# Kernel tuning notes

Hardware: AMD Instinct MI355X
Metric: run time of the kernel (lower is better)

Reference implementation:

```python
import jax, jax.numpy as jnp
import numpy as np
from jax import lax

EPS = 1e-5

def conv2d(x, w, pad):
    # x: NCHW, w: OIHW
    return lax.conv_general_dilated(x, w, (1, 1), [(pad, pad), (pad, pad)],
                                    dimension_numbers=('NCHW', 'OIHW', 'NCHW'))

def batchnorm(x, gamma, beta):
    # training-mode BN: batch statistics over N,H,W (biased variance, as torch)
    m = jnp.mean(x, axis=(0, 2, 3), keepdims=True)
    v = jnp.var(x, axis=(0, 2, 3), keepdims=True)
    g = gamma.reshape(1, -1, 1, 1)
    b = beta.reshape(1, -1, 1, 1)
    return (x - m) * jax.lax.rsqrt(v + EPS) * g + b

def setup_inputs() -> dict:
    key = jax.random.key(0)
    ks = jax.random.split(key, 8)
    B, Cin, Cmid, NC, H, W = 4, 2048, 512, 19, 64, 64
    s = lambda fan: (2.0 / fan) ** 0.5
    return {
        'x':  jax.random.normal(ks[0], (B, Cin, H, W), jnp.float32),
        'Wa': jax.random.normal(ks[1], (Cmid, Cin, 3, 3), jnp.float32) * s(Cin * 9),
        'ga': jnp.ones((Cmid,), jnp.float32),
        'ba': jnp.zeros((Cmid,), jnp.float32),
        'Wb': jax.random.normal(ks[2], (Cmid, Cmid, 1, 1), jnp.float32) * s(Cmid),
        'bb': jnp.zeros((Cmid,), jnp.float32),
        'W1': jax.random.normal(ks[3], (Cmid, Cin + Cmid, 3, 3), jnp.float32) * s((Cin + Cmid) * 9),
        'g1': jnp.ones((Cmid,), jnp.float32),
        'b1': jnp.zeros((Cmid,), jnp.float32),
        'W4': jax.random.normal(ks[4], (NC, Cmid, 1, 1), jnp.float32) * s(Cmid),
        'b4': jnp.zeros((NC,), jnp.float32),
    }

def reference(x, Wa, ga, ba, Wb, bb, W1, g1, b1, W4, b4):
    # conva: 3x3 conv (no bias) -> BN -> ReLU
    out = jax.nn.relu(batchnorm(conv2d(x, Wa, 1), ga, ba))
    # convb: 1x1 conv with bias
    out = conv2d(out, Wb, 0) + bb.reshape(1, -1, 1, 1)
    # concat input with projected features along channels
    out = jnp.concatenate([x, out], axis=1)  # [B, Cin+Cmid, H, W]
    # b1 (3x3, no bias) -> b2 BN -> b3 ReLU
    out = jax.nn.relu(batchnorm(conv2d(out, W1, 1), g1, b1))
    # b4: 1x1 classifier conv with bias
    out_final = conv2d(out, W4, 0) + b4.reshape(1, -1, 1, 1)
    return (out, out_final)
```

## Files before the change

kernel.cpp:

```cpp
#include <hip/hip_runtime.h>

typedef unsigned short ushort_t;
typedef unsigned int uint_t;
typedef unsigned long long ulong_t;

typedef __bf16 bf16x8 __attribute__((ext_vector_type(8)));
typedef float f32x4 __attribute__((ext_vector_type(4)));
typedef float f32x16 __attribute__((ext_vector_type(16)));
typedef unsigned short u16x4 __attribute__((ext_vector_type(4)));

#define DEV __device__ __forceinline__
#define SB() __builtin_amdgcn_sched_barrier(0)
#define WAITV(n) asm volatile("s_waitcnt vmcnt(" #n ")" ::: "memory")

DEV ushort_t f2bf(float x) {
  uint_t u = __float_as_uint(x);
  u += 0x7fffu + ((u >> 16) & 1u);
  return (ushort_t)(u >> 16);
}
DEV float bf2f(ushort_t h) { return __uint_as_float(((uint_t)h) << 16); }

DEV void gload16(ulong_t g, const void* l) {
  __builtin_amdgcn_global_load_lds(
      (__attribute__((address_space(1))) void*)g,
      (__attribute__((address_space(3))) void*)(void*)l,
      16, 0, 0);
}
DEV int nxt3(int x) { return x == 2 ? 0 : x + 1; }

__global__ void zero_k(float* __restrict__ p, int n) {
  int i = blockIdx.x * 256 + threadIdx.x;
  if (i < n) p[i] = 0.f;
}

__global__ __launch_bounds__(256) void cvt_x_k(const float* __restrict__ X,
                                               ushort_t* __restrict__ P) {
  __shared__ float T[64][65];
  const int t = threadIdx.x;
  const int p0 = blockIdx.x * 64;
  const int c0 = blockIdx.y * 64;
  const int b = p0 >> 12;
  const int pin0 = p0 & 4095;
#pragma unroll
  for (int it = 0; it < 4; ++it) {
    const int cl = it * 16 + (t >> 4);
    const int pl = (t & 15) * 4;
    const f32x4 v = *(const f32x4*)&X[((size_t)(b * 2048 + c0 + cl)) * 4096 + pin0 + pl];
#pragma unroll
    for (int j = 0; j < 4; ++j) T[cl][pl + j] = v[j];
  }
  __syncthreads();
#pragma unroll
  for (int it = 0; it < 4; ++it) {
    const int pl = it * 16 + (t >> 4);
    const int cl = (t & 15) * 4;
    u16x4 h, l;
#pragma unroll
    for (int j = 0; j < 4; ++j) {
      float v = T[cl + j][pl];
      ushort_t hh = f2bf(v);
      h[j] = hh;
      l[j] = f2bf(v - bf2f(hh));
    }
    const int c = c0 + cl;
    const size_t o = (size_t)(p0 + pl) * 4096 + (size_t)((c >> 5) << 6) + (c & 31);
    *(u16x4*)&P[o] = h;
    *(u16x4*)&P[o + 32] = l;
  }
}

__global__ __launch_bounds__(256) void cvt_w3n_k(const float* __restrict__ W,
                                                 ushort_t* __restrict__ P,
                                                 int I, int O) {
  const int t = threadIdx.x;
  const int o = blockIdx.y;
  const int i = blockIdx.x * 256 + t;
  const float* src = W + ((size_t)o * I + i) * 9;
  const int cb = i >> 5;
  const int kk = (i >> 4) & 1, kh = (i >> 3) & 1, e = i & 7;
  const int cg = o >> 5;
  const int lane = kh * 32 + (o & 31);
#pragma unroll
  for (int j = 0; j < 9; ++j) {
    const float v = src[j];
    const ushort_t h = f2bf(v);
    const size_t b16 = ((((size_t)(cb * 9 + j) * 16 + cg) * 2 + 0) * 2 + kk) * 64 + lane;
    P[b16 * 8 + e] = h;
    P[(b16 + 128) * 8 + e] = f2bf(v - bf2f(h));
  }
}

__global__ __launch_bounds__(256) void cvt_e_k(const float* __restrict__ W,
                                               ushort_t* __restrict__ P) {
  int i = blockIdx.x * 256 + threadIdx.x;
  float v = W[i];
  ushort_t h = f2bf(v);
  const int o = i >> 9, ic = i & 511;
  const size_t d = (size_t)o * 1024 + (size_t)((ic >> 5) << 6) + (ic & 31);
  P[d] = h;
  P[d + 32] = f2bf(v - bf2f(h));
}

__global__ __launch_bounds__(256) void stats_k(const float* __restrict__ X,
                                               float* __restrict__ S,
                                               float* __restrict__ Q) {
  const int t = threadIdx.x;
  const int r0 = blockIdx.x * 32;
  const int c = t * 2;
  float s0 = 0, s1 = 0, q0 = 0, q1 = 0;
  for (int r = 0; r < 32; ++r) {
    const float2 v = *(const float2*)&X[((size_t)(r0 + r)) * 512 + c];
    s0 += v.x; s1 += v.y;
    q0 += v.x * v.x; q1 += v.y * v.y;
  }
  atomicAdd(&S[c], s0); atomicAdd(&S[c + 1], s1);
  atomicAdd(&Q[c], q0); atomicAdd(&Q[c + 1], q1);
}

__global__ void bnparams_k(const float* __restrict__ S, const float* __restrict__ Q,
                           const float* __restrict__ g, const float* __restrict__ b,
                           float* __restrict__ sc, float* __restrict__ sh) {
  const int t = threadIdx.x;
  const float m = S[t] * (1.0f / 16384.0f);
  const float v = Q[t] * (1.0f / 16384.0f) - m * m;
  const float inv = rsqrtf(v + 1e-5f);
  const float s = g[t] * inv;
  sc[t] = s;
  sh[t] = b[t] - m * s;
}

__global__ __launch_bounds__(256) void bnact_k(const float* __restrict__ X,
                                               const float* __restrict__ sc,
                                               const float* __restrict__ sh,
                                               ushort_t* __restrict__ P) {
  const size_t i0 = ((size_t)blockIdx.x * 256 + threadIdx.x) * 16;
  const int c0 = (int)(i0 & 511);
  const size_t px = i0 >> 9;
#pragma unroll
  for (int q = 0; q < 4; ++q) {
    const f32x4 v = *(const f32x4*)&X[i0 + q * 4];
    const f32x4 s = *(const f32x4*)&sc[c0 + q * 4];
    const f32x4 d = *(const f32x4*)&sh[c0 + q * 4];
    u16x4 h, l;
#pragma unroll
    for (int j = 0; j < 4; ++j) {
      float y = fmaf(v[j], s[j], d[j]);
      y = fmaxf(y, 0.f);
      ushort_t hh = f2bf(y);
      h[j] = hh;
      l[j] = f2bf(y - bf2f(hh));
    }
    const int c = c0 + q * 4;
    const size_t o = px * 1024 + (size_t)((c >> 5) << 6) + (c & 31);
    *(u16x4*)&P[o] = h;
    *(u16x4*)&P[o + 32] = l;
  }
}

__global__ __launch_bounds__(256) void bn_nchw_k(const float* __restrict__ X,
                                                 const float* __restrict__ sc,
                                                 const float* __restrict__ sh,
                                                 float* __restrict__ O) {
  __shared__ float T[64][65];
  const int t = threadIdx.x;
  const int p0 = blockIdx.x * 64;
  const int c0 = blockIdx.y * 64;
  const int b = p0 >> 12, pin0 = p0 & 4095;
#pragma unroll
  for (int it = 0; it < 4; ++it) {
    const int pl = it * 16 + (t >> 4);
    const int cl = (t & 15) * 4;
    const f32x4 v = *(const f32x4*)&X[((size_t)(p0 + pl)) * 512 + c0 + cl];
#pragma unroll
    for (int j = 0; j < 4; ++j) {
      float y = fmaf(v[j], sc[c0 + cl + j], sh[c0 + cl + j]);
      T[pl][cl + j] = fmaxf(y, 0.f);
    }
  }
  __syncthreads();
#pragma unroll
  for (int it = 0; it < 4; ++it) {
    const int cl = it * 16 + (t >> 4);
    const int pl = (t & 15) * 4;
    f32x4 o;
#pragma unroll
    for (int j = 0; j < 4; ++j) o[j] = T[pl + j][cl];
    *(f32x4*)&O[((size_t)(b * 512 + c0 + cl)) * 4096 + pin0 + pl] = o;
  }
}

__global__ __launch_bounds__(256) void conv4_k(const float* __restrict__ X,
                                               const float* __restrict__ sc,
                                               const float* __restrict__ sh,
                                               const float* __restrict__ W4,
                                               const float* __restrict__ B4,
                                               float* __restrict__ O) {
  __shared__ float A[256][69];
  __shared__ float WL[64][19];
  const int t = threadIdx.x;
  const int g0 = blockIdx.x * 256;
  float acc[19];
#pragma unroll
  for (int n = 0; n < 19; ++n) acc[n] = 0.f;
  for (int kc = 0; kc < 8; ++kc) {
    const int k0 = kc * 64;
    __syncthreads();
#pragma unroll
    for (int it = 0; it < 16; ++it) {
      const int rl = it * 16 + (t >> 4);
      const int cl = (t & 15) * 4;
      const f32x4 v = *(const f32x4*)&X[((size_t)(g0 + rl)) * 512 + k0 + cl];
#pragma unroll
      for (int j = 0; j < 4; ++j)
        A[rl][cl + j] = fmaxf(fmaf(v[j], sc[k0 + cl + j], sh[k0 + cl + j]), 0.f);
    }
    for (int e = t; e < 1216; e += 256) {
      int k = e / 19, n = e - k * 19;
      WL[k][n] = W4[(size_t)n * 512 + k0 + k];
    }
    __syncthreads();
#pragma unroll 8
    for (int k = 0; k < 64; ++k) {
      const float a = A[t][k];
#pragma unroll
      for (int n = 0; n < 19; ++n) acc[n] = fmaf(a, WL[k][n], acc[n]);
    }
  }
  const int g = g0 + t;
  const int b = g >> 12, pin = g & 4095;
#pragma unroll
  for (int n = 0; n < 19; ++n)
    O[((size_t)(b * 19 + n)) * 4096 + pin] = acc[n] + B4[n];
}

__global__ __launch_bounds__(512, 2) void conv9dual_k(
    const ushort_t* __restrict__ A1, int S1,
    const ushort_t* __restrict__ WA, const ushort_t* __restrict__ WC,
    int CBt, const ushort_t* __restrict__ zp,
    float* __restrict__ CoA, float* __restrict__ CoC) {
  constexpr int RW = 6;
  constexpr int SPD = 24;
  constexpr int AI = 6;
  constexpr int APL = 24576;
  constexpr int ABUF = 49152;
  __shared__ char Ald[2 * ABUF];
  const int t = threadIdx.x, lane = t & 63, wid = t >> 6;
  const int wr = wid >> 1, wc = wid & 1;
  const int gid = blockIdx.x, xcd = gid & 7, k_ = gid >> 3;
  const int by = xcd * 8 + (k_ & 7), bx = k_ >> 3;
  const int b = by >> 4, r0 = (by & 15) * 4, bbase = b * 4096;
  const int pxl = lane & 31;
  const int khalf = lane >> 5;
  const int lofs = lane * 16;
  const int row0 = by * 256 + wr * 64;
  const int col0 = bx * 128 + wc * 64;
  const int rb = 4 * khalf;

  auto stageAslice = [&](int cb, int bufA, int i) {
    const int g = wid * AI + i;
    const int d = g / SPD, rem = g - d * SPD;
    const int pxb = rem >> 1, kk = rem & 1;
    const int p = pxb * 32 + pxl;
    const int irow = r0 + (p >> 6) - 1;
    const int gpx = bbase + irow * 64 + (p & 63);
    const ulong_t el = (ulong_t)gpx * (uint_t)S1 +
                       (uint_t)(cb * 64 + d * 32 + (kk * 2 + khalf) * 8);
    const bool oob = (unsigned)irow >= 64u;
    const ulong_t src = oob ? (ulong_t)(zp + lane * 8) : (ulong_t)(A1 + el);
    gload16(src, Ald + bufA + d * APL + (pxb * 2 + kk) * 1024);
  };

  struct BS { bf16x8 b[2][2][2]; };
  auto loadB = [&](BS& s, const ushort_t* W, int cs, int tap) {
#pragma unroll
    for (int ni = 0; ni < 2; ++ni)
#pragma unroll
      for (int kk = 0; kk < 2; ++kk)
#pragma unroll
        for (int dt = 0; dt < 2; ++dt) {
          const size_t b16 =
              ((((size_t)(cs * 9 + tap) * 16 + (bx * 4 + wc * 2 + ni)) * 2 + dt) * 2 + kk) * 64 + lane;
          s.b[ni][kk][dt] = *(const bf16x8*)(W + b16 * 8);
        }
  };

  f32x16 accA[2][2], accC[2][2];
#pragma unroll
  for (int i = 0; i < 2; ++i)
#pragma unroll
    for (int j2 = 0; j2 < 2; ++j2) {
      accA[i][j2] = (f32x16){0.f};
      accC[i][j2] = (f32x16){0.f};
    }

  auto mfmaBlk = [&](f32x16 (&acc)[2][2], const bf16x8 (&a)[2][2][2], const BS& s) {
    __builtin_amdgcn_s_setprio(1);
#pragma unroll
    for (int kk = 0; kk < 2; ++kk) {
#pragma unroll
      for (int mi = 0; mi < 2; ++mi)
#pragma unroll
        for (int ni = 0; ni < 2; ++ni)
          acc[mi][ni] = __builtin_amdgcn_mfma_f32_32x32x16_bf16(
              a[mi][kk][0], s.b[ni][kk][0], acc[mi][ni], 0, 0, 0);
#pragma unroll
      for (int mi = 0; mi < 2; ++mi)
#pragma unroll
        for (int ni = 0; ni < 2; ++ni)
          acc[mi][ni] = __builtin_amdgcn_mfma_f32_32x32x16_bf16(
              a[mi][kk][0], s.b[ni][kk][1], acc[mi][ni], 0, 0, 0);
#pragma unroll
      for (int mi = 0; mi < 2; ++mi)
#pragma unroll
        for (int ni = 0; ni < 2; ++ni)
          acc[mi][ni] = __builtin_amdgcn_mfma_f32_32x32x16_bf16(
              a[mi][kk][1], s.b[ni][kk][0], acc[mi][ni], 0, 0, 0);
    }
    __builtin_amdgcn_s_setprio(0);
  };

#pragma unroll
  for (int i = 0; i < AI; ++i) stageAslice(0, 0, i);
  WAITV(0);
  SB();
  __builtin_amdgcn_s_barrier();
  SB();

  for (int cs = 0; cs < CBt; ++cs) {
    const int ab = (cs & 1) * ABUF;
    const int nb = ((cs + 1) & 1) * ABUF;
#pragma unroll
    for (int tap = 0; tap < 9; ++tap) {
      BS wa;
      loadB(wa, WA, cs, tap);
      if (tap < AI && cs + 1 < CBt) stageAslice(cs + 1, nb, tap);
      const int prow = wr + tap / 3, dx = tap % 3 - 1;
      const char* Ab = Ald + ab;
      bf16x8 a[2][2][2];
#pragma unroll
      for (int mi = 0; mi < 2; ++mi) {
        const int pb0 = prow * 2 + mi;
        int ao0;
        if (dx == 0) {
          ao0 = pb0 * 2048 + lofs;
        } else {
          int px = pb0 * 32 + pxl + dx;
          px = px < 0 ? 0 : (px > RW * 64 - 1 ? RW * 64 - 1 : px);
          ao0 = (px >> 5) * 2048 + khalf * 512 + (px & 31) * 16;
        }
#pragma unroll
        for (int kk = 0; kk < 2; ++kk) {
          const int ao = ao0 + kk * 1024;
          a[mi][kk][0] = *(const bf16x8*)(Ab + ao);
          a[mi][kk][1] = *(const bf16x8*)(Ab + APL + ao);
        }
      }
      if (dx == -1 && pxl == 0) {
        bf16x8 z = {};
        a[0][0][0] = z; a[0][0][1] = z; a[0][1][0] = z; a[0][1][1] = z;
      }
      if (dx == 1 && pxl == 31) {
        bf16x8 z = {};
        a[1][0][0] = z; a[1][0][1] = z; a[1][1][0] = z; a[1][1][1] = z;
      }
      mfmaBlk(accA, a, wa);
      SB();
      BS wcs;
      loadB(wcs, WC, cs, tap);
      mfmaBlk(accC, a, wcs);
    }
    WAITV(0);
    SB();
    __builtin_amdgcn_s_barrier();
    SB();
  }

#pragma unroll
  for (int mi = 0; mi < 2; ++mi)
#pragma unroll
    for (int ni = 0; ni < 2; ++ni) {
      const int c = col0 + ni * 32 + pxl;
#pragma unroll
      for (int rg = 0; rg < 16; ++rg) {
        const int r = row0 + mi * 32 + (rg & 3) + 8 * (rg >> 2) + rb;
        CoA[(size_t)r * 512 + c] = accA[mi][ni][rg];
        CoC[(size_t)r * 512 + c] = accC[mi][ni][rg];
      }
    }
}

template <int AINIT>
__global__ __launch_bounds__(512, 2) void conv9_k(
    const ushort_t* __restrict__ A1, int S1,
    const ushort_t* __restrict__ WB, int CBt, int cbOff,
    const ushort_t* __restrict__ zp,
    float* __restrict__ Co) {
  constexpr int RW = 6;
  constexpr int SPD = 24;
  constexpr int AI = 6;
  constexpr int APL = 24576;
  constexpr int ABUF = 49152;
  __shared__ char Ald[2 * ABUF];
  const int t = threadIdx.x, lane = t & 63, wid = t >> 6;
  const int wr = wid >> 1, wc = wid & 1;
  const int gid = blockIdx.x, xcd = gid & 7, k_ = gid >> 3;
  const int by = xcd * 8 + (k_ & 7), bx = k_ >> 3;
  const int b = by >> 4, r0 = (by & 15) * 4, bbase = b * 4096;
  const int pxl = lane & 31;
  const int khalf = lane >> 5;
  const int lofs = lane * 16;
  const int row0 = by * 256 + wr * 64;
  const int col0 = bx * 128 + wc * 64;
  const int rb = 4 * khalf;

  auto stageAslice = [&](int cb, int bufA, int i) {
    const int g = wid * AI + i;
    const int d = g / SPD, rem = g - d * SPD;
    const int pxb = rem >> 1, kk = rem & 1;
    const int p = pxb * 32 + pxl;
    const int irow = r0 + (p >> 6) - 1;
    const int gpx = bbase + irow * 64 + (p & 63);
    const ulong_t el = (ulong_t)gpx * (uint_t)S1 +
                       (uint_t)(cb * 64 + d * 32 + (kk * 2 + khalf) * 8);
    const bool oob = (unsigned)irow >= 64u;
    const ulong_t src = oob ? (ulong_t)(zp + lane * 8) : (ulong_t)(A1 + el);
    gload16(src, Ald + bufA + d * APL + (pxb * 2 + kk) * 1024);
  };

  struct BS { bf16x8 b[2][2][2]; };
  auto loadB = [&](BS& s, int cs, int tap) {
#pragma unroll
    for (int ni = 0; ni < 2; ++ni)
#pragma unroll
      for (int kk = 0; kk < 2; ++kk)
#pragma unroll
        for (int dt = 0; dt < 2; ++dt) {
          const size_t b16 =
              ((((size_t)((cs + cbOff) * 9 + tap) * 16 + (bx * 4 + wc * 2 + ni)) * 2 + dt) * 2 + kk) * 64 + lane;
          s.b[ni][kk][dt] = *(const bf16x8*)(WB + b16 * 8);
        }
  };

  f32x16 acc[2][2];
  if constexpr (AINIT) {
#pragma unroll
    for (int mi = 0; mi < 2; ++mi)
#pragma unroll
      for (int ni = 0; ni < 2; ++ni) {
        const int c = col0 + ni * 32 + pxl;
#pragma unroll
        for (int rg = 0; rg < 16; ++rg) {
          const int r = row0 + mi * 32 + (rg & 3) + 8 * (rg >> 2) + rb;
          acc[mi][ni][rg] = Co[(size_t)r * 512 + c];
        }
      }
  } else {
#pragma unroll
    for (int i = 0; i < 2; ++i)
#pragma unroll
      for (int j2 = 0; j2 < 2; ++j2) acc[i][j2] = (f32x16){0.f};
  }

#pragma unroll
  for (int i = 0; i < AI; ++i) stageAslice(0, 0, i);
  WAITV(0);
  SB();
  __builtin_amdgcn_s_barrier();
  SB();

  for (int cs = 0; cs < CBt; ++cs) {
    const int ab = (cs & 1) * ABUF;
    const int nb = ((cs + 1) & 1) * ABUF;
#pragma unroll
    for (int tap = 0; tap < 9; ++tap) {
      BS wa;
      loadB(wa, cs, tap);
      if (tap < AI && cs + 1 < CBt) stageAslice(cs + 1, nb, tap);
      const int prow = wr + tap / 3, dx = tap % 3 - 1;
      const char* Ab = Ald + ab;
      bf16x8 a[2][2][2];
#pragma unroll
      for (int mi = 0; mi < 2; ++mi) {
        const int pb0 = prow * 2 + mi;
        int ao0;
        if (dx == 0) {
          ao0 = pb0 * 2048 + lofs;
        } else {
          int px = pb0 * 32 + pxl + dx;
          px = px < 0 ? 0 : (px > RW * 64 - 1 ? RW * 64 - 1 : px);
          ao0 = (px >> 5) * 2048 + khalf * 512 + (px & 31) * 16;
        }
#pragma unroll
        for (int kk = 0; kk < 2; ++kk) {
          const int ao = ao0 + kk * 1024;
          a[mi][kk][0] = *(const bf16x8*)(Ab + ao);
          a[mi][kk][1] = *(const bf16x8*)(Ab + APL + ao);
        }
      }
      if (dx == -1 && pxl == 0) {
        bf16x8 z = {};
        a[0][0][0] = z; a[0][0][1] = z; a[0][1][0] = z; a[0][1][1] = z;
      }
      if (dx == 1 && pxl == 31) {
        bf16x8 z = {};
        a[1][0][0] = z; a[1][0][1] = z; a[1][1][0] = z; a[1][1][1] = z;
      }
      __builtin_amdgcn_s_setprio(1);
#pragma unroll
      for (int kk = 0; kk < 2; ++kk) {
#pragma unroll
        for (int mi = 0; mi < 2; ++mi)
#pragma unroll
          for (int ni = 0; ni < 2; ++ni)
            acc[mi][ni] = __builtin_amdgcn_mfma_f32_32x32x16_bf16(
                a[mi][kk][0], wa.b[ni][kk][0], acc[mi][ni], 0, 0, 0);
#pragma unroll
        for (int mi = 0; mi < 2; ++mi)
#pragma unroll
          for (int ni = 0; ni < 2; ++ni)
            acc[mi][ni] = __builtin_amdgcn_mfma_f32_32x32x16_bf16(
                a[mi][kk][0], wa.b[ni][kk][1], acc[mi][ni], 0, 0, 0);
#pragma unroll
        for (int mi = 0; mi < 2; ++mi)
#pragma unroll
          for (int ni = 0; ni < 2; ++ni)
            acc[mi][ni] = __builtin_amdgcn_mfma_f32_32x32x16_bf16(
                a[mi][kk][1], wa.b[ni][kk][0], acc[mi][ni], 0, 0, 0);
      }
      __builtin_amdgcn_s_setprio(0);
    }
    WAITV(0);
    SB();
    __builtin_amdgcn_s_barrier();
    SB();
  }

#pragma unroll
  for (int mi = 0; mi < 2; ++mi)
#pragma unroll
    for (int ni = 0; ni < 2; ++ni) {
      const int c = col0 + ni * 32 + pxl;
#pragma unroll
      for (int rg = 0; rg < 16; ++rg) {
        const int r = row0 + mi * 32 + (rg & 3) + 8 * (rg >> 2) + rb;
        Co[(size_t)r * 512 + c] = acc[mi][ni][rg];
      }
    }
}

__global__ __launch_bounds__(512, 2) void conv1x1_k(
    const ushort_t* __restrict__ A1, int S1,
    const ushort_t* __restrict__ WB, int CBt, int NBS,
    const ushort_t* __restrict__ zp,
    ushort_t* __restrict__ Cp, const float* __restrict__ bias) {
  constexpr int SPD = 16;
  constexpr int AI = 4;
  constexpr int APL = 16384;
  constexpr int ABUF = 32768;
  __shared__ char lds_all[147456];
  char* Ald = lds_all;
  char* Bld = lds_all + 98304;
  const int t = threadIdx.x, lane = t & 63, wid = t >> 6;
  const int wr = wid >> 1, wc = wid & 1;
  const int gid = blockIdx.x, xcd = gid & 7, k_ = gid >> 3;
  const int by = xcd * 8 + (k_ & 7), bx = k_ >> 3;
  const int b = by >> 4, r0 = (by & 15) * 4, bbase = b * 4096;
  const int pxl = lane & 31;
  const int khalf = lane >> 5;
  const int lofs = lane * 16;

  auto stageA = [&](int cb, int bufA) {
#pragma unroll
    for (int i = 0; i < AI; ++i) {
      const int g = wid * AI + i;
      const int d = g / SPD, rem = g - d * SPD;
      const int pxb = rem >> 1, kk = rem & 1;
      const int p = pxb * 32 + pxl;
      const int irow = r0 + (p >> 6);
      const int gpx = bbase + irow * 64 + (p & 63);
      const ulong_t el = (ulong_t)gpx * (uint_t)S1 +
                         (uint_t)(cb * 64 + d * 32 + (kk * 2 + khalf) * 8);
      gload16((ulong_t)(A1 + el), Ald + bufA + d * APL + (pxb * 2 + kk) * 1024);
    }
  };
  auto stageB = [&](int cb, int bufB) {
#pragma unroll
    for (int q = 0; q < 2; ++q) {
      const int s = wid * 2 + q;
      const int d = s >> 3, rem = s & 7, cob = rem >> 1, kk = rem & 1;
      const int co = bx * 128 + cob * 32 + pxl;
      const ulong_t el = (ulong_t)co * (uint_t)NBS +
                         (uint_t)(cb * 64 + d * 32 + (kk * 2 + khalf) * 8);
      gload16((ulong_t)(WB + el), Bld + bufB + d * 8192 + (cob * 2 + kk) * 1024);
    }
  };

  f32x16 acc[2][2];
#pragma unroll
  for (int i = 0; i < 2; ++i)
#pragma unroll
    for (int j2 = 0; j2 < 2; ++j2) acc[i][j2] = (f32x16){0.f};

  auto compute = [&](int abufB, int bbufB) {
    const char* Ab = Ald + abufB;
    const char* Bb = Bld + bbufB;
    bf16x8 a[2][2][2], bf[2][2][2];
#pragma unroll
    for (int ni = 0; ni < 2; ++ni)
#pragma unroll
      for (int kk = 0; kk < 2; ++kk) {
        const int bo = (wc * 2 + ni) * 2048 + kk * 1024 + lofs;
        bf[ni][kk][0] = *(const bf16x8*)(Bb + bo);
        bf[ni][kk][1] = *(const bf16x8*)(Bb + 8192 + bo);
      }
#pragma unroll
    for (int mi = 0; mi < 2; ++mi) {
      const int ao0 = ((wr * 2 + mi)) * 2048 + lofs;
#pragma unroll
      for (int kk = 0; kk < 2; ++kk) {
        const int ao = ao0 + kk * 1024;
        a[mi][kk][0] = *(const bf16x8*)(Ab + ao);
        a[mi][kk][1] = *(const bf16x8*)(Ab + APL + ao);
      }
    }
#pragma unroll
    for (int kk = 0; kk < 2; ++kk) {
#pragma unroll
      for (int mi = 0; mi < 2; ++mi)
#pragma unroll
        for (int ni = 0; ni < 2; ++ni)
          acc[mi][ni] = __builtin_amdgcn_mfma_f32_32x32x16_bf16(
              a[mi][kk][0], bf[ni][kk][0], acc[mi][ni], 0, 0, 0);
#pragma unroll
      for (int mi = 0; mi < 2; ++mi)
#pragma unroll
        for (int ni = 0; ni < 2; ++ni)
          acc[mi][ni] = __builtin_amdgcn_mfma_f32_32x32x16_bf16(
              a[mi][kk][0], bf[ni][kk][1], acc[mi][ni], 0, 0, 0);
#pragma unroll
      for (int mi = 0; mi < 2; ++mi)
#pragma unroll
        for (int ni = 0; ni < 2; ++ni)
          acc[mi][ni] = __builtin_amdgcn_mfma_f32_32x32x16_bf16(
              a[mi][kk][1], bf[ni][kk][0], acc[mi][ni], 0, 0, 0);
    }
  };

  int rr = 0;
  stageA(0, 0);
  stageB(0, 0);
  SB();
  stageA(1, ABUF);
  stageB(1, 16384);
  for (int cs = 0; cs < CBt; ++cs) {
    SB();
    WAITV(6);
    SB();
    __builtin_amdgcn_s_barrier();
    SB();
    const int rr2 = nxt3(nxt3(rr));
    if (cs + 2 < CBt) {
      stageA(cs + 2, rr2 * ABUF);
      stageB(cs + 2, rr2 * 16384);
    }
    compute(rr * ABUF, rr * 16384);
    rr = nxt3(rr);
  }

  const int row0 = by * 256 + wr * 64;
  const int col0 = bx * 128 + wc * 64;
  const int rb = 4 * khalf;
#pragma unroll
  for (int ni = 0; ni < 2; ++ni) {
    const int c = col0 + ni * 32 + pxl;
    const float bv = bias[c];
    const size_t cg = (size_t)((c >> 5) << 6) + (c & 31);
#pragma unroll
    for (int mi = 0; mi < 2; ++mi)
#pragma unroll
      for (int rg = 0; rg < 16; ++rg) {
        const int r = row0 + mi * 32 + (rg & 3) + 8 * (rg >> 2) + rb;
        const float v = acc[mi][ni][rg] + bv;
        const ushort_t h = f2bf(v);
        Cp[(size_t)r * 1024 + cg] = h;
        Cp[(size_t)r * 1024 + cg + 32] = f2bf(v - bf2f(h));
      }
  }
}

extern "C" void kernel_launch(void* const* d_in, const int* in_sizes, int n_in,
                              void* d_out, int out_size, void* d_ws, size_t ws_size,
                              hipStream_t stream) {
  const float* x  = (const float*)d_in[0];
  const float* Wa = (const float*)d_in[1];
  const float* ga = (const float*)d_in[2];
  const float* ba = (const float*)d_in[3];
  const float* Wb = (const float*)d_in[4];
  const float* bb = (const float*)d_in[5];
  const float* W1 = (const float*)d_in[6];
  const float* g1 = (const float*)d_in[7];
  const float* b1 = (const float*)d_in[8];
  const float* W4 = (const float*)d_in[9];
  const float* b4 = (const float*)d_in[10];
  float* out0 = (float*)d_out;
  float* outF = out0 + (size_t)4 * 512 * 64 * 64;

  char* ws = (char*)d_ws;
  size_t off = 0;
  auto take = [&](size_t bytes) -> char* {
    char* p = ws + off;
    off += (bytes + 255) & ~(size_t)255;
    return p;
  };
  const size_t PAD = 16384;
  ushort_t* zp  = (ushort_t*)take(8192);
  float* sumA = (float*)take(2048);
  float* ssA  = (float*)take(2048);
  float* scA  = (float*)take(2048);
  float* shA  = (float*)take(2048);
  float* sum1 = (float*)take(2048);
  float* ss1  = (float*)take(2048);
  float* sc1  = (float*)take(2048);
  float* sh1  = (float*)take(2048);
  ushort_t* X2  = (ushort_t*)take((size_t)16384 * 4096 * 2 + PAD);
  ushort_t* WA2 = (ushort_t*)take((size_t)9 * 512 * 4096 * 2 + PAD);
  ushort_t* W12 = (ushort_t*)take((size_t)9 * 512 * 5120 * 2 + PAD);
  ushort_t* WBb = (ushort_t*)take((size_t)512 * 1024 * 2 + PAD);
  ushort_t* oA2 = (ushort_t*)take((size_t)16384 * 1024 * 2 + PAD);
  ushort_t* oB2 = (ushort_t*)take((size_t)16384 * 1024 * 2 + PAD);
  float* convaRaw = (float*)take((size_t)16384 * 512 * 4);
  float* conv1Raw = (float*)take((size_t)16384 * 512 * 4);
  if (ws_size < off) return;

  zero_k<<<dim3(24), dim3(256), 0, stream>>>((float*)ws, 6144);
  cvt_x_k<<<dim3(256, 32), dim3(256), 0, stream>>>(x, X2);
  cvt_w3n_k<<<dim3(8, 512), dim3(256), 0, stream>>>(Wa, WA2, 2048, 512);
  cvt_w3n_k<<<dim3(10, 512), dim3(256), 0, stream>>>(W1, W12, 2560, 512);
  cvt_e_k<<<dim3(1024), dim3(256), 0, stream>>>(Wb, WBb);

  conv9dual_k<<<dim3(256), dim3(512), 0, stream>>>(
      X2, 4096, WA2, W12, 64, zp, convaRaw, conv1Raw);

  stats_k<<<dim3(512), dim3(256), 0, stream>>>(convaRaw, sumA, ssA);
  bnparams_k<<<dim3(1), dim3(512), 0, stream>>>(sumA, ssA, ga, ba, scA, shA);
  bnact_k<<<dim3(2048), dim3(256), 0, stream>>>(convaRaw, scA, shA, oA2);

  conv1x1_k<<<dim3(256), dim3(512), 0, stream>>>(
      oA2, 1024, WBb, 16, 1024, zp, oB2, bb);

  conv9_k<1><<<dim3(256), dim3(512), 0, stream>>>(
      oB2, 1024, W12, 16, 64, zp, conv1Raw);

  stats_k<<<dim3(512), dim3(256), 0, stream>>>(conv1Raw, sum1, ss1);
  bnparams_k<<<dim3(1), dim3(512), 0, stream>>>(sum1, ss1, g1, b1, sc1, sh1);

  bn_nchw_k<<<dim3(256, 8), dim3(256), 0, stream>>>(conv1Raw, sc1, sh1, out0);
  conv4_k<<<dim3(64), dim3(256), 0, stream>>>(conv1Raw, sc1, sh1, W4, b4, outF);
}
```

Baseline: 1.972 ms.

## Split dual 3x3 conv reduction across two K-halves with partial-sum buffers

```diff
diff --git a/kernel.cpp b/kernel.cpp
--- a/kernel.cpp
+++ b/kernel.cpp
@@ -101,6 +101,26 @@
   P[d + 32] = f2bf(v - bf2f(h));
 }
 
+__global__ __launch_bounds__(256) void stats2_k(const float* __restrict__ X0,
+                                                const float* __restrict__ X1,
+                                                float* __restrict__ S,
+                                                float* __restrict__ Q) {
+  const int t = threadIdx.x;
+  const int r0 = blockIdx.x * 32;
+  const int c = t * 2;
+  float s0 = 0, s1 = 0, q0 = 0, q1 = 0;
+  for (int r = 0; r < 32; ++r) {
+    const size_t o = ((size_t)(r0 + r)) * 512 + c;
+    const float2 a = *(const float2*)&X0[o];
+    const float2 b = *(const float2*)&X1[o];
+    const float vx = a.x + b.x, vy = a.y + b.y;
+    s0 += vx; s1 += vy;
+    q0 += vx * vx; q1 += vy * vy;
+  }
+  atomicAdd(&S[c], s0); atomicAdd(&S[c + 1], s1);
+  atomicAdd(&Q[c], q0); atomicAdd(&Q[c + 1], q1);
+}
+
 __global__ __launch_bounds__(256) void stats_k(const float* __restrict__ X,
                                                float* __restrict__ S,
                                                float* __restrict__ Q) {
@@ -129,22 +149,24 @@
   sh[t] = b[t] - m * s;
 }
 
-__global__ __launch_bounds__(256) void bnact_k(const float* __restrict__ X,
-                                               const float* __restrict__ sc,
-                                               const float* __restrict__ sh,
-                                               ushort_t* __restrict__ P) {
+__global__ __launch_bounds__(256) void bnact2_k(const float* __restrict__ X0,
+                                                const float* __restrict__ X1,
+                                                const float* __restrict__ sc,
+                                                const float* __restrict__ sh,
+                                                ushort_t* __restrict__ P) {
   const size_t i0 = ((size_t)blockIdx.x * 256 + threadIdx.x) * 16;
   const int c0 = (int)(i0 & 511);
   const size_t px = i0 >> 9;
 #pragma unroll
   for (int q = 0; q < 4; ++q) {
-    const f32x4 v = *(const f32x4*)&X[i0 + q * 4];
+    const f32x4 v0 = *(const f32x4*)&X0[i0 + q * 4];
+    const f32x4 v1 = *(const f32x4*)&X1[i0 + q * 4];
     const f32x4 s = *(const f32x4*)&sc[c0 + q * 4];
     const f32x4 d = *(const f32x4*)&sh[c0 + q * 4];
     u16x4 h, l;
 #pragma unroll
     for (int j = 0; j < 4; ++j) {
-      float y = fmaf(v[j], s[j], d[j]);
+      float y = fmaf(v0[j] + v1[j], s[j], d[j]);
       y = fmaxf(y, 0.f);
       ushort_t hh = f2bf(y);
       h[j] = hh;
@@ -236,18 +258,19 @@
 __global__ __launch_bounds__(512, 2) void conv9dual_k(
     const ushort_t* __restrict__ A1, int S1,
     const ushort_t* __restrict__ WA, const ushort_t* __restrict__ WC,
-    int CBt, const ushort_t* __restrict__ zp,
-    float* __restrict__ CoA, float* __restrict__ CoC) {
+    const ushort_t* __restrict__ zp,
+    float* __restrict__ CoA0, float* __restrict__ CoA1,
+    float* __restrict__ CoC0, float* __restrict__ CoC1) {
   constexpr int RW = 6;
   constexpr int SPD = 24;
   constexpr int AI = 6;
   constexpr int APL = 24576;
-  constexpr int ABUF = 49152;
-  __shared__ char Ald[2 * ABUF];
+  __shared__ char Ald[49152];
   const int t = threadIdx.x, lane = t & 63, wid = t >> 6;
   const int wr = wid >> 1, wc = wid & 1;
   const int gid = blockIdx.x, xcd = gid & 7, k_ = gid >> 3;
-  const int by = xcd * 8 + (k_ & 7), bx = k_ >> 3;
+  const int by = xcd * 8 + (k_ & 7), bx = (k_ >> 3) & 3, kh = k_ >> 5;
+  const int cs0 = kh * 32, cs1 = cs0 + 32;
   const int b = by >> 4, r0 = (by & 15) * 4, bbase = b * 4096;
   const int pxl = lane & 31;
   const int khalf = lane >> 5;
@@ -255,8 +278,10 @@
   const int row0 = by * 256 + wr * 64;
   const int col0 = bx * 128 + wc * 64;
   const int rb = 4 * khalf;
-
-  auto stageAslice = [&](int cb, int bufA, int i) {
+  float* __restrict__ CoA = kh ? CoA1 : CoA0;
+  float* __restrict__ CoC = kh ? CoC1 : CoC0;
+
+  auto stageAslice = [&](int cb, int i) {
     const int g = wid * AI + i;
     const int d = g / SPD, rem = g - d * SPD;
     const int pxb = rem >> 1, kk = rem & 1;
@@ -267,7 +292,7 @@
                        (uint_t)(cb * 64 + d * 32 + (kk * 2 + khalf) * 8);
     const bool oob = (unsigned)irow >= 64u;
     const ulong_t src = oob ? (ulong_t)(zp + lane * 8) : (ulong_t)(A1 + el);
-    gload16(src, Ald + bufA + d * APL + (pxb * 2 + kk) * 1024);
+    gload16(src, Ald + d * APL + (pxb * 2 + kk) * 1024);
   };
 
   struct BS { bf16x8 b[2][2][2]; };
@@ -320,22 +345,18 @@
   };
 
 #pragma unroll
-  for (int i = 0; i < AI; ++i) stageAslice(0, 0, i);
+  for (int i = 0; i < AI; ++i) stageAslice(cs0, i);
   WAITV(0);
   SB();
   __builtin_amdgcn_s_barrier();
   SB();
 
-  for (int cs = 0; cs < CBt; ++cs) {
-    const int ab = (cs & 1) * ABUF;
-    const int nb = ((cs + 1) & 1) * ABUF;
+  for (int cs = cs0; cs < cs1; ++cs) {
 #pragma unroll
     for (int tap = 0; tap < 9; ++tap) {
       BS wa;
       loadB(wa, WA, cs, tap);
-      if (tap < AI && cs + 1 < CBt) stageAslice(cs + 1, nb, tap);
       const int prow = wr + tap / 3, dx = tap % 3 - 1;
-      const char* Ab = Ald + ab;
       bf16x8 a[2][2][2];
 #pragma unroll
       for (int mi = 0; mi < 2; ++mi) {
@@ -351,8 +372,8 @@
 #pragma unroll
         for (int kk = 0; kk < 2; ++kk) {
           const int ao = ao0 + kk * 1024;
-          a[mi][kk][0] = *(const bf16x8*)(Ab + ao);
-          a[mi][kk][1] = *(const bf16x8*)(Ab + APL + ao);
+          a[mi][kk][0] = *(const bf16x8*)(Ald + ao);
+          a[mi][kk][1] = *(const bf16x8*)(Ald + APL + ao);
         }
       }
       if (dx == -1 && pxl == 0) {
@@ -369,6 +390,13 @@
       loadB(wcs, WC, cs, tap);
       mfmaBlk(accC, a, wcs);
     }
+    SB();
+    __builtin_amdgcn_s_barrier();
+    SB();
+    if (cs + 1 < cs1) {
+#pragma unroll
+      for (int i = 0; i < AI; ++i) stageAslice(cs + 1, i);
+    }
     WAITV(0);
     SB();
     __builtin_amdgcn_s_barrier();
@@ -389,11 +417,11 @@
     }
 }
 
-template <int AINIT>
 __global__ __launch_bounds__(512, 2) void conv9_k(
     const ushort_t* __restrict__ A1, int S1,
     const ushort_t* __restrict__ WB, int CBt, int cbOff,
     const ushort_t* __restrict__ zp,
+    const float* __restrict__ P0, const float* __restrict__ P1,
     float* __restrict__ Co) {
   constexpr int RW = 6;
   constexpr int SPD = 24;
@@ -442,24 +470,17 @@
   };
 
   f32x16 acc[2][2];
-  if constexpr (AINIT) {
-#pragma unroll
-    for (int mi = 0; mi < 2; ++mi)
-#pragma unroll
-      for (int ni = 0; ni < 2; ++ni) {
-        const int c = col0 + ni * 32 + pxl;
-#pragma unroll
-        for (int rg = 0; rg < 16; ++rg) {
-          const int r = row0 + mi * 32 + (rg & 3) + 8 * (rg >> 2) + rb;
-          acc[mi][ni][rg] = Co[(size_t)r * 512 + c];
-        }
-      }
-  } else {
-#pragma unroll
-    for (int i = 0; i < 2; ++i)
-#pragma unroll
-      for (int j2 = 0; j2 < 2; ++j2) acc[i][j2] = (f32x16){0.f};
-  }
+#pragma unroll
+  for (int mi = 0; mi < 2; ++mi)
+#pragma unroll
+    for (int ni = 0; ni < 2; ++ni) {
+      const int c = col0 + ni * 32 + pxl;
+#pragma unroll
+      for (int rg = 0; rg < 16; ++rg) {
+        const int r = row0 + mi * 32 + (rg & 3) + 8 * (rg >> 2) + rb;
+        acc[mi][ni][rg] = P0[(size_t)r * 512 + c] + P1[(size_t)r * 512 + c];
+      }
+    }
 
 #pragma unroll
   for (int i = 0; i < AI; ++i) stageAslice(0, 0, i);
@@ -728,8 +749,10 @@
   ushort_t* WBb = (ushort_t*)take((size_t)512 * 1024 * 2 + PAD);
   ushort_t* oA2 = (ushort_t*)take((size_t)16384 * 1024 * 2 + PAD);
   ushort_t* oB2 = (ushort_t*)take((size_t)16384 * 1024 * 2 + PAD);
-  float* convaRaw = (float*)take((size_t)16384 * 512 * 4);
-  float* conv1Raw = (float*)take((size_t)16384 * 512 * 4);
+  float* convaP0 = (float*)take((size_t)16384 * 512 * 4);
+  float* convaP1 = (float*)take((size_t)16384 * 512 * 4);
+  float* conv1P0 = (float*)take((size_t)16384 * 512 * 4);
+  float* conv1P1 = (float*)take((size_t)16384 * 512 * 4);
   if (ws_size < off) return;
 
   zero_k<<<dim3(24), dim3(256), 0, stream>>>((float*)ws, 6144);
@@ -738,22 +761,22 @@
   cvt_w3n_k<<<dim3(10, 512), dim3(256), 0, stream>>>(W1, W12, 2560, 512);
   cvt_e_k<<<dim3(1024), dim3(256), 0, stream>>>(Wb, WBb);
 
-  conv9dual_k<<<dim3(256), dim3(512), 0, stream>>>(
-      X2, 4096, WA2, W12, 64, zp, convaRaw, conv1Raw);
-
-  stats_k<<<dim3(512), dim3(256), 0, stream>>>(convaRaw, sumA, ssA);
+  conv9dual_k<<<dim3(512), dim3(512), 0, stream>>>(
+      X2, 4096, WA2, W12, zp, convaP0, convaP1, conv1P0, conv1P1);
+
+  stats2_k<<<dim3(512), dim3(256), 0, stream>>>(convaP0, convaP1, sumA, ssA);
   bnparams_k<<<dim3(1), dim3(512), 0, stream>>>(sumA, ssA, ga, ba, scA, shA);
-  bnact_k<<<dim3(2048), dim3(256), 0, stream>>>(convaRaw, scA, shA, oA2);
+  bnact2_k<<<dim3(2048), dim3(256), 0, stream>>>(convaP0, convaP1, scA, shA, oA2);
 
   conv1x1_k<<<dim3(256), dim3(512), 0, stream>>>(
       oA2, 1024, WBb, 16, 1024, zp, oB2, bb);
 
-  conv9_k<1><<<dim3(256), dim3(512), 0, stream>>>(
-      oB2, 1024, W12, 16, 64, zp, conv1Raw);
-
-  stats_k<<<dim3(512), dim3(256), 0, stream>>>(conv1Raw, sum1, ss1);
+  conv9_k<<<dim3(256), dim3(512), 0, stream>>>(
+      oB2, 1024, W12, 16, 64, zp, conv1P0, conv1P1, conv1P0);
+
+  stats_k<<<dim3(512), dim3(256), 0, stream>>>(conv1P0, sum1, ss1);
   bnparams_k<<<dim3(1), dim3(512), 0, stream>>>(sum1, ss1, g1, b1, sc1, sh1);
 
-  bn_nchw_k<<<dim3(256, 8), dim3(256), 0, stream>>>(conv1Raw, sc1, sh1, out0);
-  conv4_k<<<dim3(64), dim3(256), 0, stream>>>(conv1Raw, sc1, sh1, W4, b4, outF);
-}
+  bn_nchw_k<<<dim3(256, 8), dim3(256), 0, stream>>>(conv1P0, sc1, sh1, out0);
+  conv4_k<<<dim3(64), dim3(256), 0, stream>>>(conv1P0, sc1, sh1, W4, b4, outF);
+}
```

Measured after the change: 1.973 ms. No clear change (+0.0%).
